# Optimization experiments

Measured on AMD Instinct MI355X. Metric: run time of the kernel, lower is better.

The kernel has to match this reference:

```python
import math
import jax, jax.numpy as jnp
import numpy as np

EPS = 1e-5
D_MODEL, N_HEADS, D_HEAD = 512, 8, 64


def make_signed_quant(num_bits):
    Qn = -2 ** (num_bits - 1)
    Qp = 2 ** (num_bits - 1) - 1

    @jax.custom_vjp
    def quant(x, alpha):
        a = jnp.maximum(alpha, EPS)
        return jnp.clip(jnp.round(x / a), Qn, Qp) * a

    def fwd(x, alpha):
        a = jnp.maximum(alpha, EPS)
        return jnp.clip(jnp.round(x / a), Qn, Qp) * a, (x, a)

    def bwd(res, g):
        x, a = res
        qw = x / a
        small = (qw < Qn).astype(g.dtype)
        big = (qw > Qp).astype(g.dtype)
        mid = 1.0 - small - big
        gs = 1.0 / math.sqrt(x.size * Qp)
        ga = jnp.sum((small * Qn + big * Qp + mid * (jnp.round(qw) - qw)) * g) * gs
        return mid * g, ga.reshape(())

    quant.defvjp(fwd, bwd)
    return quant


def make_unsigned_quant(num_bits):
    Qp = 2 ** num_bits - 1

    @jax.custom_vjp
    def quant(x, alpha):
        a = jnp.maximum(alpha, EPS)
        mn = jnp.min(x)
        return jnp.clip(jnp.round((x - mn) / a), 0, Qp) * a + mn

    def fwd(x, alpha):
        a = jnp.maximum(alpha, EPS)
        mn = jnp.min(x)
        return jnp.clip(jnp.round((x - mn) / a), 0, Qp) * a + mn, (x - mn, a)

    def bwd(res, g):
        xs, a = res
        qw = xs / a
        small = (qw < 0).astype(g.dtype)
        big = (qw > Qp).astype(g.dtype)
        mid = 1.0 - small - big
        gs = 1.0 / math.sqrt(xs.size * Qp)
        ga = jnp.sum((big * Qp + mid * (jnp.round(qw) - qw)) * g) * gs
        return mid * g, ga.reshape(())

    quant.defvjp(fwd, bwd)
    return quant


def _bwn_body(w):
    # layerwise BWN: sign(w - mean(w)) * mean(|w|)
    m = jnp.mean(jnp.abs(w))
    e = jnp.mean(w)
    return jnp.sign(w - e) * m


@jax.custom_vjp
def bwn(w):
    return _bwn_body(w)


def _bwn_fwd(w):
    return _bwn_body(w), None


def _bwn_bwd(_, g):
    return (g,)  # straight-through


bwn.defvjp(_bwn_fwd, _bwn_bwd)

sig4 = make_signed_quant(4)
sig8 = make_signed_quant(8)  # the output QuantizeLinear uses default input_bits=8
uns4 = make_unsigned_quant(4)


def layernorm(x, g, b):
    mu = jnp.mean(x, axis=-1, keepdims=True)
    var = jnp.var(x, axis=-1, keepdims=True)
    return (x - mu) / jnp.sqrt(var + 1e-5) * g + b


def attention_forward(q, k, v, Wq, Wk, Wv, Wo, bq, bk, bv, ln_g, ln_b,
                      aq_in, ak_in, av_in, a_cq, a_ck, a_cv, a_cattn, ao_in):
    B, S, _ = q.shape
    # QuantizeLinear: 4-bit elastic act quant + BWN binary weights, NO bias; then LearnableBias add
    Q = sig4(q, aq_in) @ bwn(Wq).T + bq
    K = sig4(k, ak_in) @ bwn(Wk).T + bk
    V = sig4(v, av_in) @ bwn(Wv).T + bv

    def split(x):  # [B,S,H*d] -> [B,H,S,d]
        return jnp.transpose(x.reshape(B, -1, N_HEADS, D_HEAD), (0, 2, 1, 3))

    Q, K, V = split(Q), split(K), split(V)
    Q = sig4(Q, a_cq)
    K = sig4(K, a_ck)
    V = sig4(V, a_cv)
    scores = jnp.einsum('bhqd,bhkd->bhqk', Q, K) / math.sqrt(D_HEAD)
    # NOTE: original calls scores.masked_fill(mask==0, -1e9) WITHOUT assignment,
    # so the mask has no effect on the math; replicated faithfully.
    attn = jax.nn.softmax(scores, axis=-1)
    attn = uns4(attn, a_cattn)
    ctx = jnp.einsum('bhqk,bhkd->bhqd', attn, V)
    # faithful to original `.view(B, S, H*d)` on the [B,H,S,d] tensor (no head transpose)
    ctx = ctx.reshape(B, S, N_HEADS * D_HEAD)
    out = sig8(ctx, ao_in) @ bwn(Wo).T
    return layernorm(q + out, ln_g, ln_b), scores


def setup_inputs() -> dict:
    key = jax.random.key(0)
    ks = jax.random.split(key, 8)
    B, S, D = 4, 1024, 512
    f = jnp.float32
    return {
        'q': jax.random.normal(ks[0], (B, S, D), f),
        'k': jax.random.normal(ks[1], (B, S, D), f),
        'v': jax.random.normal(ks[2], (B, S, D), f),
        'mask': jnp.ones((B, 1, S, S), jnp.int32),
        'Wq': jax.random.normal(ks[3], (D, D), f) * 0.02,
        'Wk': jax.random.normal(ks[4], (D, D), f) * 0.02,
        'Wv': jax.random.normal(ks[5], (D, D), f) * 0.02,
        'Wo': jax.random.normal(ks[6], (D, D), f) * 0.02,
        'bq': jnp.zeros((D,), f),
        'bk': jnp.zeros((D,), f),
        'bv': jnp.zeros((D,), f),
        'ln_g': jnp.ones((D,), f),
        'ln_b': jnp.zeros((D,), f),
        'aq_in': jnp.asarray(0.5, f),
        'ak_in': jnp.asarray(0.5, f),
        'av_in': jnp.asarray(0.5, f),
        'a_cq': jnp.asarray(0.2, f),
        'a_ck': jnp.asarray(0.2, f),
        'a_cv': jnp.asarray(0.2, f),
        'a_cattn': jnp.asarray(0.002, f),
        'ao_in': jnp.asarray(0.01, f),
    }


def reference(q, k, v, mask, Wq, Wk, Wv, Wo, bq, bk, bv, ln_g, ln_b,
              aq_in, ak_in, av_in, a_cq, a_ck, a_cv, a_cattn, ao_in):
    # mask is structurally unused (original masked_fill is not in-place and discarded)
    return attention_forward(q, k, v, Wq, Wk, Wv, Wo, bq, bk, bv, ln_g, ln_b,
                             aq_in, ak_in, av_in, a_cq, a_ck, a_cv, a_cattn, ao_in)
```

## Files before the change

### kernel.cpp

```cpp
#include <hip/hip_runtime.h>
#include <math.h>
#include <stdint.h>

#define EPSQ 1e-5f
#define WELEM 262144
#define OUT0N 2097152

#define O_WSUMP  0
#define O_WABSP  1024
#define O_MN     2048
#define O_COLSUM 2112
#define O_WSIGNS 16384
#define O_QLV    (O_WSIGNS + 8*WELEM)
#define O_CTXQ   O_QLV
#define O_KLV    (O_QLV + 4194304)
#define O_VLV    (O_KLV + 4194304)
#define O_KQ     (O_VLV + 4194304)
#define O_KK     (O_KQ + 4194304)
#define O_VT     (O_KK + 4194304)
#define O_RMAX   (O_VT + 4194304)
#define O_RSUM   (O_RMAX + 131072)
#define O_OUTB   (O_RSUM + 131072)

#define AS 72

typedef __bf16 bf16x8 __attribute__((ext_vector_type(8)));
typedef __bf16 bf16x4 __attribute__((ext_vector_type(4)));
typedef float  floatx4 __attribute__((ext_vector_type(4)));

struct pre2 { bf16x8 lo, hi; };
__device__ __forceinline__ pre2 ldb16(const __bf16* p) {
  pre2 r; r.lo = *(const bf16x8*)p; r.hi = *(const bf16x8*)(p + 8); return r;
}
__device__ __forceinline__ void stb16(__bf16* p, pre2 r) {
  *(bf16x8*)p = r.lo; *(bf16x8*)(p + 8) = r.hi;
}

__device__ __forceinline__ float clampf(float x, float lo, float hi) {
  return fminf(fmaxf(x, lo), hi);
}

__global__ void k_wstats(const float* Wq, const float* Wk, const float* Wv, const float* Wo,
                         float* wsum_part, float* wabs_part,
                         float* colsum, unsigned int* mnbits) {
  __shared__ float s1[256], s2[256];
  int w = blockIdx.x >> 6;
  const float* W = (w == 0) ? Wq : (w == 1) ? Wk : (w == 2) ? Wv : Wo;
  int base = (blockIdx.x & 63) * 4096;
  float s = 0.f, sa = 0.f;
  for (int i = threadIdx.x; i < 4096; i += 256) {
    float x = W[base + i];
    s += x; sa += fabsf(x);
  }
  s1[threadIdx.x] = s; s2[threadIdx.x] = sa; __syncthreads();
  for (int o = 128; o > 0; o >>= 1) {
    if (threadIdx.x < o) { s1[threadIdx.x] += s1[threadIdx.x + o]; s2[threadIdx.x] += s2[threadIdx.x + o]; }
    __syncthreads();
  }
  if (threadIdx.x == 0) { wsum_part[blockIdx.x] = s1[0]; wabs_part[blockIdx.x] = s2[0]; }
  if (blockIdx.x == 0) {
    for (int i = threadIdx.x; i < 2048; i += 256) colsum[i] = 0.f;
    if (threadIdx.x == 0) mnbits[0] = 0x7f800000u;
  }
}

__global__ __launch_bounds__(256) void k_signqx(
    const float* Wq, const float* Wk, const float* Wv, const float* Wo,
    const float* wsum_part,
    const float* q, const float* kin, const float* vin,
    const float* aq, const float* ak, const float* av,
    __bf16* wsigns, __bf16* qlv, __bf16* klv, __bf16* vlv) {
  int y = blockIdx.y;
  if (y == 0) {
    int idx = (blockIdx.x * 256 + threadIdx.x) * 4;
    int w = idx >> 18;
    const float* W = (w == 0) ? Wq : (w == 1) ? Wk : (w == 2) ? Wv : Wo;
    float s = 0.f;
#pragma unroll
    for (int i = 0; i < 64; ++i) s += wsum_part[w * 64 + i];
    float e = s * (1.0f / 262144.0f);
    float4 x = *(const float4*)&W[idx & (WELEM - 1)];
    bf16x4 o = { (__bf16)(float)((x.x > e) - (x.x < e)),
                 (__bf16)(float)((x.y > e) - (x.y < e)),
                 (__bf16)(float)((x.z > e) - (x.z < e)),
                 (__bf16)(float)((x.w > e) - (x.w < e)) };
    *(bf16x4*)&wsigns[idx] = o;
  } else {
    int z = y - 1;
    const float* X = (z == 0) ? q : (z == 1) ? kin : vin;
    const float* ap = (z == 0) ? aq : (z == 1) ? ak : av;
    __bf16* O = (z == 0) ? qlv : (z == 1) ? klv : vlv;
    float a = fmaxf(ap[0], EPSQ);
    size_t i = ((size_t)blockIdx.x * 256 + threadIdx.x) * 8;
    float4 x0 = *(const float4*)&X[i];
    float4 x1 = *(const float4*)&X[i + 4];
    bf16x8 o = { (__bf16)clampf(rintf(x0.x / a), -8.f, 7.f),
                 (__bf16)clampf(rintf(x0.y / a), -8.f, 7.f),
                 (__bf16)clampf(rintf(x0.z / a), -8.f, 7.f),
                 (__bf16)clampf(rintf(x0.w / a), -8.f, 7.f),
                 (__bf16)clampf(rintf(x1.x / a), -8.f, 7.f),
                 (__bf16)clampf(rintf(x1.y / a), -8.f, 7.f),
                 (__bf16)clampf(rintf(x1.z / a), -8.f, 7.f),
                 (__bf16)clampf(rintf(x1.w / a), -8.f, 7.f) };
    *(bf16x8*)&O[i] = o;
  }
}

__global__ __launch_bounds__(256) void k_proj(
    const __bf16* qlv, const __bf16* klv, const __bf16* vlv,
    const float* bq, const float* bk, const float* bv,
    const float* aq, const float* ak, const float* av,
    const float* acq, const float* ack, const float* acv,
    const __bf16* wsigns, const float* wabs_part,
    __bf16* kqo, __bf16* kko, __bf16* vto, float* colsum) {
  __shared__ __align__(16) __bf16 As[64][AS];
  __shared__ __align__(16) __bf16 Bs[64][AS];
  int z = blockIdx.z;
  const __bf16* X   = (z == 0) ? qlv : (z == 1) ? klv : vlv;
  const float* bias = (z == 0) ? bq  : (z == 1) ? bk  : bv;
  const float* aip  = (z == 0) ? aq  : (z == 1) ? ak  : av;
  const float* ahp  = (z == 0) ? acq : (z == 1) ? ack : acv;
  float a_in = fmaxf(aip[0], EPSQ);
  float a_hd = fmaxf(ahp[0], EPSQ);
  float sa = 0.f;
#pragma unroll
  for (int i = 0; i < 64; ++i) sa += wabs_part[z * 64 + i];
  float m_w  = sa * (1.0f / 262144.0f);
  const __bf16* S = wsigns + (size_t)z * WELEM;

  int n0 = blockIdx.x * 64;
  int f0 = blockIdx.y * 64;
  int t = threadIdx.x;
  int lane = t & 63, w = t >> 6, quad = lane >> 4, l16 = lane & 15;
  int e16 = (t & 3) * 16, mrow = t >> 2;
  const __bf16* ap = &X[(size_t)(n0 + mrow) * 512 + e16];
  const __bf16* bp = &S[(size_t)(f0 + mrow) * 512 + e16];
  floatx4 acc[4];
#pragma unroll
  for (int nt = 0; nt < 4; ++nt) acc[nt] = (floatx4){0.f, 0.f, 0.f, 0.f};

  pre2 pa = ldb16(ap), pb = ldb16(bp);
  for (int k0 = 0; k0 < 512; k0 += 64) {
    if (k0) __syncthreads();
    stb16(&As[mrow][e16], pa);
    stb16(&Bs[mrow][e16], pb);
    if (k0 + 64 < 512) { pa = ldb16(ap + k0 + 64); pb = ldb16(bp + k0 + 64); }
    __syncthreads();
#pragma unroll
    for (int kh = 0; kh < 64; kh += 32) {
      bf16x8 a = *(const bf16x8*)&As[w * 16 + l16][kh + quad * 8];
#pragma unroll
      for (int nt = 0; nt < 4; ++nt) {
        bf16x8 b = *(const bf16x8*)&Bs[nt * 16 + l16][kh + quad * 8];
        acc[nt] = __builtin_amdgcn_mfma_f32_16x16x32_bf16(a, b, acc[nt], 0, 0, 0);
      }
    }
  }
  float s_am = a_in * m_w;
  if (z != 2) {
    __bf16* outp = (z == 0) ? kqo : kko;
#pragma unroll
    for (int nt = 0; nt < 4; ++nt) {
      int f = f0 + nt * 16 + l16;
      int h = f >> 6, dd = f & 63;
      float bia = bias[f];
#pragma unroll
      for (int r = 0; r < 4; ++r) {
        int n = n0 + w * 16 + quad * 4 + r;
        int b = n >> 10, srow = n & 1023;
        float P = s_am * acc[nt][r] + bia;
        float hq = clampf(rintf(P / a_hd), -8.f, 7.f);
        outp[(size_t)((b * 8 + h) * 1024 + srow) * 64 + dd] = (__bf16)hq;
      }
    }
  } else {
    int b = n0 >> 10;
    int srow0 = (n0 & 1023) + w * 16 + quad * 4;
#pragma unroll
    for (int nt = 0; nt < 4; ++nt) {
      int f = f0 + nt * 16 + l16;
      int h = f >> 6, dd = f & 63;
      int bh = b * 8 + h;
      float bia = bias[f];
      float part = 0.f;
      bf16x4 pack;
#pragma unroll
      for (int r = 0; r < 4; ++r) {
        float P = s_am * acc[nt][r] + bia;
        float hq = clampf(rintf(P / a_hd), -8.f, 7.f);
        pack[r] = (__bf16)hq;
        part += hq;
      }
      *(bf16x4*)&vto[((size_t)bh * 64 + dd) * 1024 + srow0] = pack;
      atomicAdd(&colsum[bh * 64 + dd], part);
    }
  }
}

__global__ __launch_bounds__(256) void k_qks(
    const __bf16* kq, const __bf16* kkv,
    const float* acq, const float* ack,
    float* scores, float* rmax, float* rsum, unsigned int* mnbits) {
  __shared__ __align__(16) __bf16 As[64][AS];
  __shared__ __align__(16) __bf16 Bs[64][AS];
  __shared__ float redmin[16];
  int bh = blockIdx.y;
  int q0 = blockIdx.x * 64;
  const __bf16* A  = kq  + (size_t)bh * 65536;
  const __bf16* Bp = kkv + (size_t)bh * 65536;
  float* Sp = scores + ((size_t)bh * 1024 + q0) * 1024;
  int t = threadIdx.x;
  int lane = t & 63, w = t >> 6, quad = lane >> 4, l16 = lane & 15;
  int e16 = (t & 3) * 16, mrow = t >> 2;
  float sc = fmaxf(acq[0], EPSQ) * fmaxf(ack[0], EPSQ) * 0.125f;

  stb16(&As[mrow][e16], ldb16(&A[(q0 + mrow) * 64 + e16]));
  float m_run[4], l_run[4], mn_run[4];
#pragma unroll
  for (int rr = 0; rr < 4; ++rr) { m_run[rr] = -INFINITY; l_run[rr] = 0.f; mn_run[rr] = INFINITY; }

  pre2 pb = ldb16(&Bp[mrow * 64 + e16]);
  for (int ct = 0; ct < 16; ++ct) {
    if (ct) __syncthreads();
    stb16(&Bs[mrow][e16], pb);
    if (ct < 15) pb = ldb16(&Bp[((ct + 1) * 64 + mrow) * 64 + e16]);
    __syncthreads();
    floatx4 acc[4];
#pragma unroll
    for (int nt = 0; nt < 4; ++nt) acc[nt] = (floatx4){0.f, 0.f, 0.f, 0.f};
#pragma unroll
    for (int kh = 0; kh < 64; kh += 32) {
      bf16x8 a = *(const bf16x8*)&As[w * 16 + l16][kh + quad * 8];
#pragma unroll
      for (int nt = 0; nt < 4; ++nt) {
        bf16x8 b = *(const bf16x8*)&Bs[nt * 16 + l16][kh + quad * 8];
        acc[nt] = __builtin_amdgcn_mfma_f32_16x16x32_bf16(a, b, acc[nt], 0, 0, 0);
      }
    }
#pragma unroll
    for (int rr = 0; rr < 4; ++rr) {
      int row = w * 16 + quad * 4 + rr;
      float v[4];
#pragma unroll
      for (int nt = 0; nt < 4; ++nt) {
        v[nt] = sc * acc[nt][rr];
        Sp[(size_t)row * 1024 + ct * 64 + nt * 16 + l16] = v[nt];
      }
      float tmax = fmaxf(fmaxf(v[0], v[1]), fmaxf(v[2], v[3]));
      float tmin = fminf(fminf(v[0], v[1]), fminf(v[2], v[3]));
      mn_run[rr] = fminf(mn_run[rr], tmin);
      float mnew = fmaxf(m_run[rr], tmax);
      float s = 0.f;
#pragma unroll
      for (int nt = 0; nt < 4; ++nt) s += expf(v[nt] - mnew);
      l_run[rr] = l_run[rr] * expf(m_run[rr] - mnew) + s;
      m_run[rr] = mnew;
    }
  }
#pragma unroll
  for (int o = 1; o < 16; o <<= 1) {
#pragma unroll
    for (int rr = 0; rr < 4; ++rr) {
      float mo = __shfl_xor(m_run[rr], o);
      float lo = __shfl_xor(l_run[rr], o);
      float mnew = fmaxf(m_run[rr], mo);
      l_run[rr] = l_run[rr] * expf(m_run[rr] - mnew) + lo * expf(mo - mnew);
      m_run[rr] = mnew;
      mn_run[rr] = fminf(mn_run[rr], __shfl_xor(mn_run[rr], o));
    }
  }
  if (l16 == 0) {
    float cand = INFINITY;
#pragma unroll
    for (int rr = 0; rr < 4; ++rr) {
      int r = bh * 1024 + q0 + w * 16 + quad * 4 + rr;
      rmax[r] = m_run[rr];
      rsum[r] = l_run[rr];
      cand = fminf(cand, expf(mn_run[rr] - m_run[rr]) * (1.0f / l_run[rr]));
    }
    redmin[w * 4 + quad] = cand;
  }
  __syncthreads();
  if (t == 0) {
    float c = redmin[0];
#pragma unroll
    for (int i = 1; i < 16; ++i) c = fminf(c, redmin[i]);
    atomicMin(mnbits, __float_as_uint(c));
  }
}

__global__ __launch_bounds__(256) void k_pv(
    const __bf16* kq, const __bf16* kkv,
    const float* rmax, const float* rsum,
    const float* mnf, const float* colsum, const __bf16* vt,
    const float* acq, const float* ack,
    const float* acattn, const float* acv, const float* ao,
    __bf16* ctxq) {
  __shared__ __align__(16) __bf16 Ks[64][AS];
  __shared__ __align__(16) __bf16 Vs[64][AS];
  __shared__ __align__(16) __bf16 As[32][AS];
  int bh = blockIdx.y;
  int m0 = blockIdx.x * 32;
  float mn    = mnf[0];
  float a_att = fmaxf(acattn[0], EPSQ);
  float a_v   = fmaxf(acv[0], EPSQ);
  float a_o   = fmaxf(ao[0], EPSQ);
  float sc    = fmaxf(acq[0], EPSQ) * fmaxf(ack[0], EPSQ) * 0.125f;
  const __bf16* Qp = kq  + (size_t)bh * 65536;
  const __bf16* Kp = kkv + (size_t)bh * 65536;
  const __bf16* Vt = vt  + (size_t)bh * 65536;
  int t = threadIdx.x;
  int lane = t & 63, w = t >> 6, quad = lane >> 4, l16 = lane & 15;
  int e16 = (t & 3) * 16, mrow = t >> 2;
  int mt = w & 1, np = w >> 1;

  bf16x8 qa[2][2];
#pragma unroll
  for (int mh = 0; mh < 2; ++mh)
#pragma unroll
    for (int kh2 = 0; kh2 < 2; ++kh2)
      qa[mh][kh2] = *(const bf16x8*)&Qp[(size_t)(m0 + mh * 16 + l16) * 64 + kh2 * 32 + quad * 8];

  float rm[2][4], inv[2][4];
#pragma unroll
  for (int mh = 0; mh < 2; ++mh)
#pragma unroll
    for (int r = 0; r < 4; ++r) {
      int rr = bh * 1024 + m0 + mh * 16 + quad * 4 + r;
      rm[mh][r]  = rmax[rr];
      inv[mh][r] = 1.0f / rsum[rr];
    }

  floatx4 acc[2];
  acc[0] = (floatx4){0.f, 0.f, 0.f, 0.f};
  acc[1] = (floatx4){0.f, 0.f, 0.f, 0.f};

  pre2 kpre = ldb16(&Kp[(size_t)mrow * 64 + e16]);
  pre2 vpre = ldb16(&Vt[(size_t)mrow * 1024 + e16]);
  for (int ct = 0; ct < 16; ++ct) {
    if (ct) __syncthreads();
    stb16(&Ks[mrow][e16], kpre);
    stb16(&Vs[mrow][e16], vpre);
    if (ct < 15) {
      kpre = ldb16(&Kp[(size_t)((ct + 1) * 64 + mrow) * 64 + e16]);
      vpre = ldb16(&Vt[(size_t)mrow * 1024 + (ct + 1) * 64 + e16]);
    }
    __syncthreads();
    floatx4 s2[2];
    s2[0] = (floatx4){0.f, 0.f, 0.f, 0.f};
    s2[1] = (floatx4){0.f, 0.f, 0.f, 0.f};
#pragma unroll
    for (int kh2 = 0; kh2 < 2; ++kh2) {
      bf16x8 b = *(const bf16x8*)&Ks[w * 16 + l16][kh2 * 32 + quad * 8];
#pragma unroll
      for (int mh = 0; mh < 2; ++mh)
        s2[mh] = __builtin_amdgcn_mfma_f32_16x16x32_bf16(qa[mh][kh2], b, s2[mh], 0, 0, 0);
    }
#pragma unroll
    for (int mh = 0; mh < 2; ++mh)
#pragma unroll
      for (int r = 0; r < 4; ++r) {
        float p = expf(sc * s2[mh][r] - rm[mh][r]) * inv[mh][r];
        As[mh * 16 + quad * 4 + r][w * 16 + l16] =
            (__bf16)clampf(rintf((p - mn) / a_att), 0.f, 15.f);
      }
    __syncthreads();
#pragma unroll
    for (int kh = 0; kh < 64; kh += 32) {
      bf16x8 a = *(const bf16x8*)&As[mt * 16 + l16][kh + quad * 8];
#pragma unroll
      for (int j = 0; j < 2; ++j) {
        bf16x8 b = *(const bf16x8*)&Vs[(np * 2 + j) * 16 + l16][kh + quad * 8];
        acc[j] = __builtin_amdgcn_mfma_f32_16x16x32_bf16(a, b, acc[j], 0, 0, 0);
      }
    }
  }
  float scf = a_att * a_v;
  float mnv = mn * a_v;
  int b = bh >> 3, h = bh & 7;
#pragma unroll
  for (int j = 0; j < 2; ++j) {
    int dd = (np * 2 + j) * 16 + l16;
    float cs = colsum[bh * 64 + dd];
#pragma unroll
    for (int r = 0; r < 4; ++r) {
      int srow = m0 + mt * 16 + quad * 4 + r;
      float ctx = scf * acc[j][r] + mnv * cs;
      float c8 = clampf(rintf(ctx / a_o), -128.f, 127.f);
      ctxq[(size_t)b * 524288 + (size_t)(h * 128 + (srow >> 3)) * 512 + (srow & 7) * 64 + dd] = (__bf16)c8;
    }
  }
}

__global__ __launch_bounds__(256) void k_outg(
    const __bf16* ctxq, const __bf16* signs_o,
    const float* wabs_part, const float* ao, float* outb) {
  __shared__ __align__(16) __bf16 As[64][AS];
  __shared__ __align__(16) __bf16 Bs[64][AS];
  int n0 = blockIdx.x * 64, f0 = blockIdx.y * 64;
  int t = threadIdx.x;
  int lane = t & 63, w = t >> 6, quad = lane >> 4, l16 = lane & 15;
  int e16 = (t & 3) * 16, mrow = t >> 2;
  const __bf16* ap = &ctxq[(size_t)(n0 + mrow) * 512 + e16];
  const __bf16* bp = &signs_o[(size_t)(f0 + mrow) * 512 + e16];
  floatx4 acc[4];
#pragma unroll
  for (int nt = 0; nt < 4; ++nt) acc[nt] = (floatx4){0.f, 0.f, 0.f, 0.f};
  pre2 pa = ldb16(ap), pb = ldb16(bp);
  for (int k0 = 0; k0 < 512; k0 += 64) {
    if (k0) __syncthreads();
    stb16(&As[mrow][e16], pa);
    stb16(&Bs[mrow][e16], pb);
    if (k0 + 64 < 512) { pa = ldb16(ap + k0 + 64); pb = ldb16(bp + k0 + 64); }
    __syncthreads();
#pragma unroll
    for (int kh = 0; kh < 64; kh += 32) {
      bf16x8 a = *(const bf16x8*)&As[w * 16 + l16][kh + quad * 8];
#pragma unroll
      for (int nt = 0; nt < 4; ++nt) {
        bf16x8 b = *(const bf16x8*)&Bs[nt * 16 + l16][kh + quad * 8];
        acc[nt] = __builtin_amdgcn_mfma_f32_16x16x32_bf16(a, b, acc[nt], 0, 0, 0);
      }
    }
  }
  float sa = 0.f;
#pragma unroll
  for (int i = 0; i < 64; ++i) sa += wabs_part[3 * 64 + i];
  float scale = fmaxf(ao[0], EPSQ) * (sa * (1.0f / 262144.0f));
#pragma unroll
  for (int nt = 0; nt < 4; ++nt)
#pragma unroll
    for (int r = 0; r < 4; ++r)
      outb[(size_t)(n0 + w * 16 + quad * 4 + r) * 512 + f0 + nt * 16 + l16] = scale * acc[nt][r];
}

__global__ __launch_bounds__(256) void k_ln(
    const float* q, const float* outb, const float* g, const float* bb, float* out0) {
  __shared__ float red[256];
  int r = blockIdx.x, t = threadIdx.x;
  const float* qp = q + (size_t)r * 512;
  const float* op = outb + (size_t)r * 512;
  float y0 = qp[t] + op[t];
  float y1 = qp[t + 256] + op[t + 256];
  red[t] = y0 + y1; __syncthreads();
  for (int o = 128; o > 0; o >>= 1) { if (t < o) red[t] += red[t + o]; __syncthreads(); }
  float mu = red[0] * (1.0f / 512.0f); __syncthreads();
  float d0 = y0 - mu, d1 = y1 - mu;
  red[t] = d0 * d0 + d1 * d1; __syncthreads();
  for (int o = 128; o > 0; o >>= 1) { if (t < o) red[t] += red[t + o]; __syncthreads(); }
  float var = red[0] * (1.0f / 512.0f);
  float den = sqrtf(var + 1e-5f);
  out0[(size_t)r * 512 + t]       = d0 / den * g[t] + bb[t];
  out0[(size_t)r * 512 + t + 256] = d1 / den * g[t + 256] + bb[t + 256];
}

extern "C" void kernel_launch(void* const* d_in, const int* in_sizes, int n_in,
                              void* d_out, int out_size, void* d_ws, size_t ws_size,
                              hipStream_t stream) {
  const float* q   = (const float*)d_in[0];
  const float* k   = (const float*)d_in[1];
  const float* v   = (const float*)d_in[2];
  const float* Wq  = (const float*)d_in[4];
  const float* Wk  = (const float*)d_in[5];
  const float* Wv  = (const float*)d_in[6];
  const float* Wo  = (const float*)d_in[7];
  const float* bq  = (const float*)d_in[8];
  const float* bk  = (const float*)d_in[9];
  const float* bv  = (const float*)d_in[10];
  const float* lng = (const float*)d_in[11];
  const float* lnb = (const float*)d_in[12];
  const float* aq  = (const float*)d_in[13];
  const float* ak  = (const float*)d_in[14];
  const float* av  = (const float*)d_in[15];
  const float* acq = (const float*)d_in[16];
  const float* ack = (const float*)d_in[17];
  const float* acv = (const float*)d_in[18];
  const float* aca = (const float*)d_in[19];
  const float* ao  = (const float*)d_in[20];

  char* ws = (char*)d_ws;
  float*  wsum_p = (float*)(ws + O_WSUMP);
  float*  wabs_p = (float*)(ws + O_WABSP);
  float*  mnf    = (float*)(ws + O_MN);
  float*  colsum = (float*)(ws + O_COLSUM);
  __bf16* wsigns = (__bf16*)(ws + O_WSIGNS);
  __bf16* qlv    = (__bf16*)(ws + O_QLV);
  __bf16* klv    = (__bf16*)(ws + O_KLV);
  __bf16* vlv    = (__bf16*)(ws + O_VLV);
  __bf16* kqb    = (__bf16*)(ws + O_KQ);
  __bf16* kkb    = (__bf16*)(ws + O_KK);
  __bf16* vtb    = (__bf16*)(ws + O_VT);
  float*  rmax   = (float*)(ws + O_RMAX);
  float*  rsum   = (float*)(ws + O_RSUM);
  __bf16* ctxq   = (__bf16*)(ws + O_CTXQ);
  float*  outb   = (float*)(ws + O_OUTB);

  float* out0   = (float*)d_out;
  float* scores = (float*)d_out + OUT0N;

  k_wstats<<<256, 256, 0, stream>>>(Wq, Wk, Wv, Wo, wsum_p, wabs_p, colsum,
                                    (unsigned int*)mnf);
  k_signqx<<<dim3(1024, 4), 256, 0, stream>>>(Wq, Wk, Wv, Wo, wsum_p,
                                              q, k, v, aq, ak, av,
                                              wsigns, qlv, klv, vlv);
  k_proj<<<dim3(64, 8, 3), 256, 0, stream>>>(qlv, klv, vlv, bq, bk, bv, aq, ak, av,
                                             acq, ack, acv, wsigns, wabs_p,
                                             kqb, kkb, vtb, colsum);
  k_qks<<<dim3(16, 32), 256, 0, stream>>>(kqb, kkb, acq, ack, scores, rmax, rsum,
                                          (unsigned int*)mnf);
  k_pv<<<dim3(32, 32), 256, 0, stream>>>(kqb, kkb, rmax, rsum, mnf, colsum, vtb,
                                         acq, ack, aca, acv, ao, ctxq);
  k_outg<<<dim3(64, 8), 256, 0, stream>>>(ctxq, wsigns + 3 * WELEM, wabs_p, ao, outb);
  k_ln<<<4096, 256, 0, stream>>>(q, outb, lng, lnb, out0);
}
```

Before: 337.2 us.

## Fuse LayerNorm into output projection via last-block counter; nontemporal score stores

Removes the separate LayerNorm kernel. Each output-projection block adds the residual q into outb, and the last of the 8 column blocks for a row tile, detected with an atomic counter and thread fences, normalises those 64 rows and writes the final output. This saves one launch and the separate residual read pass. The trade-off is that only 64 of the 512 blocks do the LN work, and the variance now uses E[x^2]-mu^2, which is less numerically stable. The large score matrix is also written with nontemporal stores to reduce cache pollution.

Result: slower. 411.2 us (+22.0%).

```diff
diff --git a/kernel.cpp b/kernel.cpp
--- a/kernel.cpp
+++ b/kernel.cpp
@@ -10,6 +10,7 @@
 #define O_WABSP  1024
 #define O_MN     2048
 #define O_COLSUM 2112
+#define O_CNT    10304
 #define O_WSIGNS 16384
 #define O_QLV    (O_WSIGNS + 8*WELEM)
 #define O_CTXQ   O_QLV
@@ -42,7 +43,7 @@
 
 __global__ void k_wstats(const float* Wq, const float* Wk, const float* Wv, const float* Wo,
                          float* wsum_part, float* wabs_part,
-                         float* colsum, unsigned int* mnbits) {
+                         float* colsum, unsigned int* mnbits, unsigned int* cnt) {
   __shared__ float s1[256], s2[256];
   int w = blockIdx.x >> 6;
   const float* W = (w == 0) ? Wq : (w == 1) ? Wk : (w == 2) ? Wv : Wo;
@@ -60,6 +61,7 @@
   if (threadIdx.x == 0) { wsum_part[blockIdx.x] = s1[0]; wabs_part[blockIdx.x] = s2[0]; }
   if (blockIdx.x == 0) {
     for (int i = threadIdx.x; i < 2048; i += 256) colsum[i] = 0.f;
+    if (threadIdx.x < 64) cnt[threadIdx.x] = 0u;
     if (threadIdx.x == 0) mnbits[0] = 0x7f800000u;
   }
 }
@@ -244,7 +246,7 @@
 #pragma unroll
       for (int nt = 0; nt < 4; ++nt) {
         v[nt] = sc * acc[nt][rr];
-        Sp[(size_t)row * 1024 + ct * 64 + nt * 16 + l16] = v[nt];
+        __builtin_nontemporal_store(v[nt], &Sp[(size_t)row * 1024 + ct * 64 + nt * 16 + l16]);
       }
       float tmax = fmaxf(fmaxf(v[0], v[1]), fmaxf(v[2], v[3]));
       float tmin = fminf(fminf(v[0], v[1]), fminf(v[2], v[3]));
@@ -394,9 +396,12 @@
 
 __global__ __launch_bounds__(256) void k_outg(
     const __bf16* ctxq, const __bf16* signs_o,
-    const float* wabs_part, const float* ao, float* outb) {
+    const float* wabs_part, const float* ao,
+    const float* q, const float* lng, const float* lnb,
+    float* outb, unsigned int* cnt, float* out0) {
   __shared__ __align__(16) __bf16 As[64][AS];
   __shared__ __align__(16) __bf16 Bs[64][AS];
+  __shared__ unsigned int oldc;
   int n0 = blockIdx.x * 64, f0 = blockIdx.y * 64;
   int t = threadIdx.x;
   int lane = t & 63, w = t >> 6, quad = lane >> 4, l16 = lane & 15;
@@ -430,28 +435,46 @@
 #pragma unroll
   for (int nt = 0; nt < 4; ++nt)
 #pragma unroll
-    for (int r = 0; r < 4; ++r)
-      outb[(size_t)(n0 + w * 16 + quad * 4 + r) * 512 + f0 + nt * 16 + l16] = scale * acc[nt][r];
-}
-
-__global__ __launch_bounds__(256) void k_ln(
-    const float* q, const float* outb, const float* g, const float* bb, float* out0) {
-  __shared__ float red[256];
-  int r = blockIdx.x, t = threadIdx.x;
-  const float* qp = q + (size_t)r * 512;
-  const float* op = outb + (size_t)r * 512;
-  float y0 = qp[t] + op[t];
-  float y1 = qp[t + 256] + op[t + 256];
-  red[t] = y0 + y1; __syncthreads();
-  for (int o = 128; o > 0; o >>= 1) { if (t < o) red[t] += red[t + o]; __syncthreads(); }
-  float mu = red[0] * (1.0f / 512.0f); __syncthreads();
-  float d0 = y0 - mu, d1 = y1 - mu;
-  red[t] = d0 * d0 + d1 * d1; __syncthreads();
-  for (int o = 128; o > 0; o >>= 1) { if (t < o) red[t] += red[t + o]; __syncthreads(); }
-  float var = red[0] * (1.0f / 512.0f);
+    for (int r = 0; r < 4; ++r) {
+      size_t idx = (size_t)(n0 + w * 16 + quad * 4 + r) * 512 + f0 + nt * 16 + l16;
+      outb[idx] = q[idx] + scale * acc[nt][r];
+    }
+  __threadfence();
+  __syncthreads();
+  if (t == 0) oldc = atomicAdd(&cnt[blockIdx.x], 1);
+  __syncthreads();
+  if (oldc != 7) return;
+  __threadfence();
+  int r0 = n0 + (t >> 2);
+  int qd = t & 3;
+  const float* yp = outb + (size_t)r0 * 512 + qd * 128;
+  float s = 0.f, s2 = 0.f;
+#pragma unroll
+  for (int i = 0; i < 128; i += 4) {
+    float4 v4 = *(const float4*)&yp[i];
+    s  += v4.x + v4.y + v4.z + v4.w;
+    s2 += v4.x * v4.x + v4.y * v4.y + v4.z * v4.z + v4.w * v4.w;
+  }
+  s  += __shfl_xor(s, 1);  s  += __shfl_xor(s, 2);
+  s2 += __shfl_xor(s2, 1); s2 += __shfl_xor(s2, 2);
+  float mu  = s * (1.0f / 512.0f);
+  float var = s2 * (1.0f / 512.0f) - mu * mu;
   float den = sqrtf(var + 1e-5f);
-  out0[(size_t)r * 512 + t]       = d0 / den * g[t] + bb[t];
-  out0[(size_t)r * 512 + t + 256] = d1 / den * g[t + 256] + bb[t + 256];
+  float* op = out0 + (size_t)r0 * 512 + qd * 128;
+  const float* gp = lng + qd * 128;
+  const float* bbp = lnb + qd * 128;
+#pragma unroll
+  for (int i = 0; i < 128; i += 4) {
+    float4 v4 = *(const float4*)&yp[i];
+    float4 g4 = *(const float4*)&gp[i];
+    float4 b4 = *(const float4*)&bbp[i];
+    float4 o;
+    o.x = (v4.x - mu) / den * g4.x + b4.x;
+    o.y = (v4.y - mu) / den * g4.y + b4.y;
+    o.z = (v4.z - mu) / den * g4.z + b4.z;
+    o.w = (v4.w - mu) / den * g4.w + b4.w;
+    *(float4*)&op[i] = o;
+  }
 }
 
 extern "C" void kernel_launch(void* const* d_in, const int* in_sizes, int n_in,
@@ -483,6 +506,7 @@
   float*  wabs_p = (float*)(ws + O_WABSP);
   float*  mnf    = (float*)(ws + O_MN);
   float*  colsum = (float*)(ws + O_COLSUM);
+  unsigned int* cnt = (unsigned int*)(ws + O_CNT);
   __bf16* wsigns = (__bf16*)(ws + O_WSIGNS);
   __bf16* qlv    = (__bf16*)(ws + O_QLV);
   __bf16* klv    = (__bf16*)(ws + O_KLV);
@@ -499,7 +523,7 @@
   float* scores = (float*)d_out + OUT0N;
 
   k_wstats<<<256, 256, 0, stream>>>(Wq, Wk, Wv, Wo, wsum_p, wabs_p, colsum,
-                                    (unsigned int*)mnf);
+                                    (unsigned int*)mnf, cnt);
   k_signqx<<<dim3(1024, 4), 256, 0, stream>>>(Wq, Wk, Wv, Wo, wsum_p,
                                               q, k, v, aq, ak, av,
                                               wsigns, qlv, klv, vlv);
@@ -510,6 +534,6 @@
                                           (unsigned int*)mnf);
   k_pv<<<dim3(32, 32), 256, 0, stream>>>(kqb, kkb, rmax, rsum, mnf, colsum, vtb,
                                          acq, ack, aca, acv, ao, ctxq);
-  k_outg<<<dim3(64, 8), 256, 0, stream>>>(ctxq, wsigns + 3 * WELEM, wabs_p, ao, outb);
-  k_ln<<<4096, 256, 0, stream>>>(q, outb, lng, lnb, out0);
-}
+  k_outg<<<dim3(64, 8), 256, 0, stream>>>(ctxq, wsigns + 3 * WELEM, wabs_p, ao,
+                                          q, lng, lnb, outb, cnt, out0);
+}
```
